# Optimization experiments

Hardware: AMD Instinct MI355X
Metric: run time of the kernel (lower is better)

## Reference

```python
import jax, jax.numpy as jnp
import numpy as np

# SSD post-process constants (mirror torch module init args)
V0, V1 = 0.1, 0.2            # box coder variances
SCORE_THRESH = 0.05
NMS_THRESH = 0.45
DET_PER_IMG = 100
MIN_SIZE = 0.01
PRE_NMS_TOPK = 1000          # padded candidate budget for jit-safe NMS


def setup_inputs() -> dict:
    key = jax.random.key(0)
    k1, k2, k3 = jax.random.split(key, 3)
    B, P, C = 32, 24564, 81
    pred_logits = jax.random.normal(k1, (B, P, C), dtype=jnp.float32)
    pred_boxes = jax.random.normal(k2, (B, P, 4), dtype=jnp.float32)
    # priors in (cx, cy, w, h), normalized coords
    u = jax.random.uniform(k3, (P, 4), dtype=jnp.float32)
    priors = jnp.concatenate([u[:, :2], 0.02 + 0.3 * u[:, 2:]], axis=-1)
    target_sizes = 512.0 * jnp.ones((B, 2), dtype=jnp.float32)  # (h, w)
    return {"pred_logits": pred_logits, "pred_boxes": pred_boxes,
            "priors": priors, "target_sizes": target_sizes}


def _decode(rel, priors):
    # SSD box decode: priors are cxcywh, rel codes scaled by variances -> xyxy
    xy = priors[:, :2] + rel[:, :2] * V0 * priors[:, 2:]
    wh = priors[:, 2:] * jnp.exp(rel[:, 2:] * V1)
    return jnp.concatenate([xy - wh / 2, xy + wh / 2], axis=-1)


def _box_iou(a, b):
    area_a = (a[:, 2] - a[:, 0]) * (a[:, 3] - a[:, 1])
    area_b = (b[:, 2] - b[:, 0]) * (b[:, 3] - b[:, 1])
    lt = jnp.maximum(a[:, None, :2], b[None, :, :2])
    rb = jnp.minimum(a[:, None, 2:], b[None, :, 2:])
    wh = jnp.clip(rb - lt, 0.0)
    inter = wh[..., 0] * wh[..., 1]
    return inter / (area_a[:, None] + area_b[None, :] - inter + 1e-12)


def _per_image(logits, rel, priors, tsize):
    P, C = logits.shape
    boxes = _decode(rel, priors)                       # [P,4] xyxy
    scale = jnp.tile(tsize[::-1], 2)                   # (w,h,w,h) = flip(0).repeat(2)
    boxes = boxes * scale
    scores = jax.nn.softmax(logits, axis=-1)[:, 1:]    # drop background, [P,C-1]
    size_ok = ((boxes[:, 2] - boxes[:, 0]) >= MIN_SIZE) & \
              ((boxes[:, 3] - boxes[:, 1]) >= MIN_SIZE)
    masked = jnp.where((scores > SCORE_THRESH) & size_ok[:, None], scores, -1.0)
    top_s, top_i = jax.lax.top_k(masked.reshape(-1), PRE_NMS_TOPK)
    prior_i = top_i // (C - 1)
    cls0 = top_i % (C - 1)                             # label - 1
    b = boxes[prior_i]                                 # [K,4]
    valid = top_s > SCORE_THRESH
    # batched_nms: offset boxes by class so different classes never overlap
    maxc = jnp.max(jnp.where(valid[:, None], b, 0.0))
    bo = b + (cls0.astype(b.dtype) * (maxc + 1.0))[:, None]
    ious = jax.lax.stop_gradient(_box_iou(bo, bo))
    K = PRE_NMS_TOPK
    idx = jnp.arange(K)

    def body(i, keep):
        sup = jnp.any(keep & (idx < i) & (ious[i] > NMS_THRESH))
        return keep.at[i].set(keep[i] & ~sup)

    keep = jax.lax.fori_loop(0, K, body, valid)
    kept_s = jnp.where(keep, top_s, -1.0)
    fs, fi = jax.lax.top_k(kept_s, DET_PER_IMG)        # keep order == score order
    fb = b[fi]
    fl = cls0[fi] + 1
    fvalid = fs > SCORE_THRESH
    fb = jnp.where(fvalid[:, None], fb, 0.0)
    fl = jnp.where(fvalid, fl, -1)
    fs = jnp.where(fvalid, fs, 0.0)
    return fb, fs, fl, fvalid


def reference(pred_logits, pred_boxes, priors, target_sizes):
    # Returns padded per-image detections: boxes [B,100,4], scores [B,100],
    # labels [B,100] (int, -1 = padding), valid mask [B,100].
    return jax.vmap(_per_image, in_axes=(0, 0, None, 0))(
        pred_logits, pred_boxes, priors, target_sizes)
```

## Files before the change

kernel.cpp:

```cpp
#include <hip/hip_runtime.h>
#include <stdint.h>

typedef unsigned int u32;
typedef unsigned long long u64;
typedef long long i64;

#define NCLS 81
#define KTOP 1000
#define DETS 100
#define CANDCAP 2048
#define BIGCAP 131072
#define TPB 256
#define RCH 64
#define NCH 4
#define CNT_STRIDE 32
#define FBINS 4096

__device__ __forceinline__ double fast_exp(double x)
{
    const double LOG2E = 1.4426950408889634074;
    const double LN2HI = 6.93147180369123816490e-01;
    const double LN2LO = 1.90821492927058770002e-10;
    double nf = rint(x * LOG2E);
    int n = (int)nf;
    double r = fma(-nf, LN2HI, x);
    r = fma(-nf, LN2LO, r);
    double p = 2.7557319223985893e-06;
    p = fma(p, r, 2.4801587301587302e-05);
    p = fma(p, r, 1.9841269841269841e-04);
    p = fma(p, r, 1.3888888888888889e-03);
    p = fma(p, r, 8.3333333333333332e-03);
    p = fma(p, r, 4.1666666666666664e-02);
    p = fma(p, r, 1.6666666666666666e-01);
    p = fma(p, r, 5.0000000000000000e-01);
    p = fma(p, r, 1.0);
    p = fma(p, r, 1.0);
    i64 bits = ((i64)(n + 1023)) << 52;
    return p * __longlong_as_double(bits);
}

__global__ __launch_bounds__(TPB, 5)
void score_kernel(const float* __restrict__ logits, const float* __restrict__ rel,
                  const float* __restrict__ priors, const float* __restrict__ ts,
                  int P, u64* __restrict__ bigCand, u32* __restrict__ bigCnt)
{
    __shared__ float xs[RCH * NCLS];
    __shared__ double sden[RCH];
    __shared__ float tfl[RCH];
    __shared__ u32 okm[RCH];
    __shared__ u32 wsum[4];
    __shared__ u32 s_base;
    int img = blockIdx.y;
    int p0 = blockIdx.x * TPB;
    int tid = threadIdx.x;
    int lane = tid & 63, wid = tid >> 6;
    int sub = tid & 3;
    int rloc = tid >> 2;

    for (int ch = 0; ch < NCH; ++ch) {
        int rbase = p0 + ch * RCH;
        __syncthreads();
        int nrows = min(RCH, P - rbase);
        if (nrows == RCH) {
            const float4* s4 = (const float4*)(logits + ((size_t)img * P + rbase) * NCLS);
            float4* d4 = (float4*)xs;
#pragma unroll
            for (int k = 0; k < 5; ++k) d4[k * TPB + tid] = s4[k * TPB + tid];
            if (tid < 16) d4[5 * TPB + tid] = s4[5 * TPB + tid];
        } else if (nrows > 0) {
            const float* s1 = logits + ((size_t)img * P + rbase) * NCLS;
            int nflat = nrows * NCLS;
            for (int f = tid; f < nflat; f += TPB) xs[f] = s1[f];
        }
        __syncthreads();

        int p = rbase + rloc;
        bool live = (p < P);
        const float* row = xs + rloc * NCLS;

        float vals[21];
#pragma unroll
        for (int i = 0; i < 21; ++i) {
            int j = sub + 4 * i;
            vals[i] = (live && j < NCLS) ? row[j] : -1.0e30f;
        }

        float m = vals[0];
#pragma unroll
        for (int i = 1; i < 21; ++i) m = fmaxf(m, vals[i]);
        m = fmaxf(m, __shfl_xor(m, 1));
        m = fmaxf(m, __shfl_xor(m, 2));

        double md = (double)m;
        double acc = 0.0;
#pragma unroll
        for (int i = 0; i < 21; ++i) {
            if (vals[i] > -1.0e29f)
                acc += fast_exp((double)vals[i] - md);
        }
        acc += __shfl_xor(acc, 1);
        acc += __shfl_xor(acc, 2);
        double s = acc;
        if (sub == 0) sden[rloc] = s;
        __syncthreads();

        if (tid < RCH) {
            int p2 = rbase + tid;
            bool ok2 = false;
            float t2 = 3.4e38f;
            if (p2 < P) {
                double s2 = sden[tid];
                t2 = logf(0.05f * (float)s2) - 3e-4f;
                const float* rp = rel + ((size_t)img * P + p2) * 4;
                const float* pp = priors + (size_t)p2 * 4;
                double pw = pp[2], ph = pp[3];
                double cx = (double)pp[0] + (double)rp[0] * 0.1 * pw;
                double cy = (double)pp[1] + (double)rp[1] * 0.1 * ph;
                double bw = pw * fast_exp((double)rp[2] * 0.2);
                double bh = ph * fast_exp((double)rp[3] * 0.2);
                double sw = (double)ts[img * 2 + 1], sh = (double)ts[img * 2 + 0];
                double x1 = (cx - bw * 0.5) * sw, x2 = (cx + bw * 0.5) * sw;
                double y1 = (cy - bh * 0.5) * sh, y2 = (cy + bh * 0.5) * sh;
                ok2 = (x2 - x1 >= 0.01) && (y2 - y1 >= 0.01);
            }
            okm[tid] = ok2 ? 1u : 0u;
            tfl[tid] = t2;
        }
        __syncthreads();
        bool ok = okm[rloc] != 0;
        float tf_lo = tfl[rloc];

        u32 cnt = 0;
#pragma unroll
        for (int i = 0; i < 21; ++i) {
            int j = sub + 4 * i;
            if (ok && j != 0 && vals[i] - m > tf_lo) cnt++;
        }
        u32 inc = cnt;
        for (int off = 1; off < 64; off <<= 1) {
            u32 v = __shfl_up(inc, off);
            if (lane >= off) inc += v;
        }
        if (lane == 63) wsum[wid] = inc;
        __syncthreads();
        if (tid == 0) {
            u32 tot = wsum[0] + wsum[1] + wsum[2] + wsum[3];
            s_base = tot ? atomicAdd(&bigCnt[(size_t)img * CNT_STRIDE], tot) : 0u;
        }
        __syncthreads();
        if (ok && cnt) {
            u32 wbase = 0;
            for (int w = 0; w < wid; ++w) wbase += wsum[w];
            u32 pos = s_base + wbase + inc - cnt;
#pragma unroll
            for (int i = 0; i < 21; ++i) {
                int j = sub + 4 * i;
                if (j != 0 && vals[i] - m > tf_lo) {
                    double e = fast_exp((double)vals[i] - md);
                    double sc = e / s;
                    u64 entry = 0ULL;
                    if (sc > 0.05) {
                        u32 key = __float_as_uint((float)sc) ^ 0x80000000u;
                        u32 idx = (u32)p * 80u + (u32)(j - 1);
                        entry = ((u64)key << 32) | (u64)(u32)(~idx);
                    }
                    if (pos < BIGCAP)
                        bigCand[(size_t)img * BIGCAP + pos] = entry;
                    pos++;
                }
            }
        }
    }
}

__global__ __launch_bounds__(1024)
void select_nms_kernel(const u64* __restrict__ bigCand, const u32* __restrict__ bigCnt,
                       const float* __restrict__ rel, const float* __restrict__ priors,
                       const float* __restrict__ ts, int P,
                       float* __restrict__ out, int B)
{
    __shared__ u64 smemU[7584];
    __shared__ u32 s_sel, s_run, s_floor, s_cnt;
    int img = blockIdx.x;
    int tid = threadIdx.x;
    int lane = tid & 63;
    u32 bc = bigCnt[(size_t)img * CNT_STRIDE];
    if (bc > (u32)BIGCAP) bc = BIGCAP;
    const u64* src = bigCand + (size_t)img * BIGCAP;

    u64* s = smemU;
    u32* h = (u32*)((char*)smemU + 16384);

    for (int i = tid; i < FBINS; i += 1024) h[i] = 0;
    if (tid == 0) s_cnt = 0;
    __syncthreads();
    for (u32 k = tid; k < bc; k += 1024) {
        u32 key = (u32)(src[k] >> 32);
        if (key) atomicAdd(&h[key >> 20], 1u);
    }
    __syncthreads();
    if (tid == 0) {
        u32 run = 0; int d = FBINS - 1;
        for (; d >= 0; --d) {
            if (run + h[d] >= KTOP) break;
            run += h[d];
        }
        s_sel = (u32)d;
        s_run = run;
    }
    __syncthreads();
    u32 d12 = s_sel;
    if ((int)d12 >= 0) {
        u32 run0 = s_run;
        if (tid < 16) h[tid] = 0;
        __syncthreads();
        for (u32 k = tid; k < bc; k += 1024) {
            u32 key = (u32)(src[k] >> 32);
            if (key && (key >> 20) == d12) atomicAdd(&h[(key >> 16) & 0xF], 1u);
        }
        __syncthreads();
        if (tid == 0) {
            u32 run = run0;
            int b = 15;
            for (; b >= 0; --b) {
                run += h[b];
                if (run >= KTOP) break;
            }
            if (b < 0) b = 0;
            s_floor = ((d12 << 4) | (u32)b) << 16;
        }
    } else {
        if (tid == 0) s_floor = 0u;
    }
    __syncthreads();
    u32 fkey = s_floor;
    for (u32 k0 = 0; k0 < bc; k0 += 1024) {
        u32 k = k0 + tid;
        u64 e = 0; bool pass = false;
        if (k < bc) {
            e = src[k];
            u32 ky = (u32)(e >> 32);
            pass = ky && (ky >= fkey);
        }
        u64 mask = __ballot(pass);
        if (mask) {
            int leader = __ffsll((long long)mask) - 1;
            u32 basePos = 0;
            if (lane == leader) basePos = atomicAdd(&s_cnt, (u32)__popcll(mask));
            basePos = __shfl(basePos, leader);
            if (pass) {
                u32 pos = basePos + (u32)__popcll(mask & ((1ULL << lane) - 1ULL));
                if (pos < CANDCAP) s[pos] = e;
            }
        }
    }
    __syncthreads();
    u32 n = s_cnt; if (n > CANDCAP) n = CANDCAP;
    for (int k = tid; k < CANDCAP; k += 1024)
        if ((u32)k >= n) s[k] = 0ULL;
    __syncthreads();
    for (u32 len = 2; len <= CANDCAP; len <<= 1) {
        for (u32 j = len >> 1; j > 0; j >>= 1) {
            for (int i = tid; i < CANDCAP; i += 1024) {
                u32 ixj = (u32)i ^ j;
                if (ixj > (u32)i) {
                    u64 a = s[i], b = s[ixj];
                    bool up = ((i & len) == 0);
                    if (up ? (a < b) : (a > b)) { s[i] = b; s[ixj] = a; }
                }
            }
            __syncthreads();
        }
    }

    u64 e = (tid < KTOP) ? s[tid] : 0ULL;
    __syncthreads();

    double* o0   = (double*)smemU;
    double* o1   = (double*)((char*)smemU +  8000);
    double* o2   = (double*)((char*)smemU + 16000);
    double* o3   = (double*)((char*)smemU + 24000);
    double* arA  = (double*)((char*)smemU + 32000);
    u32*    dead = (u32*)   ((char*)smemU + 40000);
    int*    clsA = (int*)   ((char*)smemU + 44000);
    float*  scA  = (float*) ((char*)smemU + 48000);
    int*    keptS= (int*)   ((char*)smemU + 52000);
    double* red  = (double*)((char*)smemU + 52416);

    double b0 = 0, b1 = 0, b2 = 0, b3 = 0;
    int cls = 0;
    float score = -1.0f;
    bool validE = (tid < KTOP) && ((e >> 32) != 0ULL);
    double v = -1e300;
    if (tid < KTOP) {
        if (validE) {
            u32 key = (u32)(e >> 32);
            score = __uint_as_float(key ^ 0x80000000u);
            u32 idx = ~((u32)e);
            int p = (int)(idx / 80u), c0 = (int)(idx % 80u);
            cls = c0;
            const float* rp = rel + ((size_t)img * P + p) * 4;
            const float* pp = priors + (size_t)p * 4;
            double pw = pp[2], ph = pp[3];
            double cx = (double)pp[0] + (double)rp[0] * 0.1 * pw;
            double cy = (double)pp[1] + (double)rp[1] * 0.1 * ph;
            double bw = pw * fast_exp((double)rp[2] * 0.2);
            double bh = ph * fast_exp((double)rp[3] * 0.2);
            double sw = (double)ts[img * 2 + 1], sh = (double)ts[img * 2 + 0];
            b0 = (cx - bw * 0.5) * sw; b1 = (cy - bh * 0.5) * sh;
            b2 = (cx + bw * 0.5) * sw; b3 = (cy + bh * 0.5) * sh;
            v = fmax(fmax(b0, b1), fmax(b2, b3));
        } else {
            v = 0.0;
        }
        o0[tid] = b0; o1[tid] = b1; o2[tid] = b2; o3[tid] = b3;
        dead[tid] = validE ? 0u : 1u;
        clsA[tid] = cls; scA[tid] = score;
        red[tid] = v;
    } else {
        red[tid] = -1e300;
    }
    __syncthreads();
    for (int off = 512; off > 0; off >>= 1) {
        if (tid < off) red[tid] = fmax(red[tid], red[tid + off]);
        __syncthreads();
    }
    double maxc1 = red[0] + 1.0;
    if (tid < KTOP) {
        double off_ = (double)cls * maxc1;
        double a0 = b0 + off_, a1 = b1 + off_, a2 = b2 + off_, a3 = b3 + off_;
        arA[tid] = (a2 - a0) * (a3 - a1);
    }
    __syncthreads();

    int cnt = 0, i = 0;
    while (cnt < DETS) {
        while (i < KTOP && dead[i]) ++i;
        if (i >= KTOP) break;
        if (tid == 0) keptS[cnt] = i;
        cnt++;
        double offi = (double)clsA[i] * maxc1;
        double a0 = o0[i] + offi, a1 = o1[i] + offi;
        double a2 = o2[i] + offi, a3 = o3[i] + offi;
        double aA = arA[i];
        int j = tid;
        if (j < KTOP && j > i && !dead[j]) {
            double offj = (double)clsA[j] * maxc1;
            double c0 = o0[j] + offj, c1 = o1[j] + offj;
            double c2 = o2[j] + offj, c3 = o3[j] + offj;
            double ltx = fmax(a0, c0), lty = fmax(a1, c1);
            double rbx = fmin(a2, c2), rby = fmin(a3, c3);
            double wx = fmax(rbx - ltx, 0.0), wy = fmax(rby - lty, 0.0);
            double inter = wx * wy;
            if (inter > 0.45 * (((aA + arA[j]) - inter) + 1e-12)) dead[j] = 1;
        }
        ++i;
        __syncthreads();
    }
    __syncthreads();

    int r = tid;
    if (r < DETS) {
        float f0 = 0.f, f1 = 0.f, f2 = 0.f, f3 = 0.f, sc = 0.f, lb = -1.0f, vd = 0.f;
        if (r < cnt) {
            int i2 = keptS[r];
            f0 = (float)o0[i2]; f1 = (float)o1[i2];
            f2 = (float)o2[i2]; f3 = (float)o3[i2];
            sc = scA[i2];
            lb = (float)(clsA[i2] + 1);
            vd = 1.0f;
        }
        ((float4*)out)[(size_t)img * DETS + r] = make_float4(f0, f1, f2, f3);
        out[(size_t)B * 400 + (size_t)img * DETS + r] = sc;
        out[(size_t)B * 500 + (size_t)img * DETS + r] = lb;
        out[(size_t)B * 600 + (size_t)img * DETS + r] = vd;
    }
}

extern "C" void kernel_launch(void* const* d_in, const int* in_sizes, int n_in,
                              void* d_out, int out_size, void* d_ws, size_t ws_size,
                              hipStream_t stream)
{
    const float* logits = (const float*)d_in[0];
    const float* rel    = (const float*)d_in[1];
    const float* priors = (const float*)d_in[2];
    const float* ts     = (const float*)d_in[3];
    float* out = (float*)d_out;
    int P = in_sizes[2] / 4;
    int B = in_sizes[3] / 2;

    char* ws = (char*)d_ws;
    size_t zero_bytes = (size_t)B * CNT_STRIDE * 4;
    size_t o_big = (zero_bytes + 255) & ~(size_t)255;

    u32* bigCnt  = (u32*)ws;
    u64* bigCand = (u64*)(ws + o_big);

    hipMemsetAsync(ws, 0, zero_bytes, stream);

    dim3 g1((P + TPB - 1) / TPB, B);
    score_kernel<<<g1, TPB, 0, stream>>>(logits, rel, priors, ts, P, bigCand, bigCnt);
    select_nms_kernel<<<B, 1024, 0, stream>>>(bigCand, bigCnt, rel, priors, ts, P,
                                              out, B);
    (void)n_in; (void)out_size; (void)ws_size;
}
```

Measured before the change: 333.8 us.

## Replace NMS dead array scan with wavefront ballot bitmask and raise score occupancy

The greedy NMS loop no longer keeps a per-candidate dead flag array in shared memory that every thread scans linearly to find the next survivor. Each wavefront now ballots its suppression results into a 64-bit word, the first wave holds 16 alive-mask words, and the next survivor is found with ffs over ballots. This removes the serial scan and the scattered dead-flag writes but adds a second barrier per iteration. The score kernel's launch bound also rises from 5 to 7 blocks per CU, which may limit registers and cause spills.

```diff
diff --git a/kernel.cpp b/kernel.cpp
--- a/kernel.cpp
+++ b/kernel.cpp
@@ -39,7 +39,7 @@
     return p * __longlong_as_double(bits);
 }
 
-__global__ __launch_bounds__(TPB, 5)
+__global__ __launch_bounds__(TPB, 7)
 void score_kernel(const float* __restrict__ logits, const float* __restrict__ rel,
                   const float* __restrict__ priors, const float* __restrict__ ts,
                   int P, u64* __restrict__ bigCand, u32* __restrict__ bigCnt)
@@ -180,10 +180,13 @@
                        float* __restrict__ out, int B)
 {
     __shared__ u64 smemU[7584];
+    __shared__ u64 supW16[16];
     __shared__ u32 s_sel, s_run, s_floor, s_cnt;
+    __shared__ int s_i;
     int img = blockIdx.x;
     int tid = threadIdx.x;
     int lane = tid & 63;
+    int wv = tid >> 6;
     u32 bc = bigCnt[(size_t)img * CNT_STRIDE];
     if (bc > (u32)BIGCAP) bc = BIGCAP;
     const u64* src = bigCand + (size_t)img * BIGCAP;
@@ -281,7 +284,6 @@
     double* o2   = (double*)((char*)smemU + 16000);
     double* o3   = (double*)((char*)smemU + 24000);
     double* arA  = (double*)((char*)smemU + 32000);
-    u32*    dead = (u32*)   ((char*)smemU + 40000);
     int*    clsA = (int*)   ((char*)smemU + 44000);
     float*  scA  = (float*) ((char*)smemU + 48000);
     int*    keptS= (int*)   ((char*)smemU + 52000);
@@ -314,7 +316,6 @@
             v = 0.0;
         }
         o0[tid] = b0; o1[tid] = b1; o2[tid] = b2; o3[tid] = b3;
-        dead[tid] = validE ? 0u : 1u;
         clsA[tid] = cls; scA[tid] = score;
         red[tid] = v;
     } else {
@@ -331,31 +332,52 @@
         double a0 = b0 + off_, a1 = b1 + off_, a2 = b2 + off_, a3 = b3 + off_;
         arA[tid] = (a2 - a0) * (a3 - a1);
     }
-    __syncthreads();
-
-    int cnt = 0, i = 0;
+    u64 wb = __ballot(validE);
+    if (lane == 0) supW16[wv] = wb;
+    __syncthreads();
+    u64 aliveW = (tid < 16) ? supW16[tid] : 0ULL;
+
+    int cnt = 0;
     while (cnt < DETS) {
-        while (i < KTOP && dead[i]) ++i;
-        if (i >= KTOP) break;
+        if (wv == 0) {
+            bool has = (lane < 16) && (aliveW != 0ULL);
+            u64 bal = __ballot(has);
+            int ni = -1;
+            if (bal) {
+                int w0 = __ffsll((i64)bal) - 1;
+                u64 word = __shfl(aliveW, w0);
+                int bt = __ffsll((i64)word) - 1;
+                ni = w0 * 64 + bt;
+            }
+            if (lane == 0) s_i = ni;
+        }
+        __syncthreads();
+        int i = s_i;
+        if (i < 0) break;
         if (tid == 0) keptS[cnt] = i;
         cnt++;
         double offi = (double)clsA[i] * maxc1;
         double a0 = o0[i] + offi, a1 = o1[i] + offi;
         double a2 = o2[i] + offi, a3 = o3[i] + offi;
         double aA = arA[i];
-        int j = tid;
-        if (j < KTOP && j > i && !dead[j]) {
-            double offj = (double)clsA[j] * maxc1;
-            double c0 = o0[j] + offj, c1 = o1[j] + offj;
-            double c2 = o2[j] + offj, c3 = o3[j] + offj;
+        bool sup = false;
+        if (tid < KTOP && tid > i) {
+            double offj = (double)clsA[tid] * maxc1;
+            double c0 = o0[tid] + offj, c1 = o1[tid] + offj;
+            double c2 = o2[tid] + offj, c3 = o3[tid] + offj;
             double ltx = fmax(a0, c0), lty = fmax(a1, c1);
             double rbx = fmin(a2, c2), rby = fmin(a3, c3);
             double wx = fmax(rbx - ltx, 0.0), wy = fmax(rby - lty, 0.0);
             double inter = wx * wy;
-            if (inter > 0.45 * (((aA + arA[j]) - inter) + 1e-12)) dead[j] = 1;
-        }
-        ++i;
-        __syncthreads();
+            sup = inter > 0.45 * (((aA + arA[tid]) - inter) + 1e-12);
+        }
+        u64 ws = __ballot(sup);
+        if (lane == 0) supW16[wv] = ws;
+        __syncthreads();
+        if (tid < 16) {
+            aliveW &= ~supW16[tid];
+            if (tid == (i >> 6)) aliveW &= ~(1ULL << (i & 63));
+        }
     }
     __syncthreads();
 
```

Measured after the change: 352.3 us. +5.5%, slower.
